# Kernel tuning notes

Hardware: AMD Instinct MI355X
Metric: run time of the kernel (lower is better)

The kernel has to match this reference:

```python
import jax, jax.numpy as jnp
import numpy as np
from jax.scipy.special import logsumexp

S, L = 32768, 512  # seq_len, label_num


def setup_inputs() -> dict:
    key = jax.random.key(0)
    k1, k2, k3 = jax.random.split(key, 3)
    logit = jax.random.normal(k1, (S, L), dtype=jnp.float32)   # emissions [S, L]
    labels = jax.random.randint(k2, (S,), 0, L)                # gold path [S]
    T = jax.random.normal(k3, (L, L), dtype=jnp.float32)       # T[next, prev]
    return {"logit": logit, "labels": labels, "T": T}


def _crf_loss(logit, T, labels):
    # Forward algorithm: alpha_t[j] = logsumexp_i(alpha_{t-1}[i] + T[j, i]) + feat_t[j]
    alpha0 = logit[0]

    def step(alpha, feat):
        new_alpha = logsumexp(alpha[None, :] + T, axis=1) + feat  # [L]
        return new_alpha, None

    alpha_final, _ = jax.lax.scan(step, alpha0, logit[1:])
    log_Z = logsumexp(alpha_final)

    # Gold path score: feat_0[y0] + sum_{t>0} (feat_t[y_t] + T[y_t, y_{t-1}])
    emit = logit[0, labels[0]] + jnp.sum(logit[jnp.arange(1, logit.shape[0]), labels[1:]])
    trans = jnp.sum(T[labels[1:], labels[:-1]])
    gold = emit + trans
    return log_Z - gold


def reference(logit, labels, T):
    return _crf_loss(logit, T, labels)
```

## Files before the change

kernel.cpp:

```cpp
#include <hip/hip_runtime.h>
#include <stdint.h>


#define S_LEN 32768
#define L 512
#define CH 16
#define NCF 2048
#define NB  256
#define LN448 6.104793232f
#define LN2   0.6931471806f

#define OFF_EAF  0
#define OFF_EAB  (256*1024)
#define OFF_G    (512*1024)
#define OFF_H    (OFF_G + 2048*512*2)
#define OFF_LSE  (OFF_H + 2048*512*2)
#define OFF_GOLD (OFF_LSE + 4104*4)
#define OFF_BAR  (OFF_GOLD + 1024)

typedef float v4f __attribute__((ext_vector_type(4)));

__device__ __forceinline__ float b2f(unsigned short u){
  return __uint_as_float(((unsigned)u) << 16);
}
__device__ __forceinline__ unsigned short f2b(float x){
  unsigned u = __float_as_uint(x);
  return (unsigned short)((u + 0x7fffu + ((u >> 16) & 1u)) >> 16);
}
__device__ __forceinline__ unsigned char to_fp8(float v){
  int u = __builtin_amdgcn_cvt_pk_fp8_f32(v, v, 0, false);
  return (unsigned char)(u & 0xff);
}

__device__ __forceinline__ void stg_u8(unsigned char* p, unsigned char v){
  __hip_atomic_store(p, v, __ATOMIC_RELAXED, __HIP_MEMORY_SCOPE_AGENT);
}
__device__ __forceinline__ void stg_u64(unsigned long long* p, unsigned long long v){
  __hip_atomic_store(p, v, __ATOMIC_RELAXED, __HIP_MEMORY_SCOPE_AGENT);
}
__device__ __forceinline__ void stg_f32(float* p, float v){
  __hip_atomic_store(p, v, __ATOMIC_RELAXED, __HIP_MEMORY_SCOPE_AGENT);
}

__device__ __forceinline__ void grid_bar(unsigned* bar, unsigned target){
  __syncthreads();
  if (threadIdx.x == 0) {
    __hip_atomic_fetch_add(bar, 1u, __ATOMIC_RELAXED, __HIP_MEMORY_SCOPE_AGENT);
    unsigned it = 0;
    while (__hip_atomic_load(bar, __ATOMIC_RELAXED, __HIP_MEMORY_SCOPE_AGENT) < target) {
      __builtin_amdgcn_s_sleep(8);
      if ((++it & 255u) == 0u)
        (void)__hip_atomic_load(bar, __ATOMIC_ACQUIRE, __HIP_MEMORY_SCOPE_AGENT);
    }
    __builtin_amdgcn_fence(__ATOMIC_ACQUIRE, "agent");
  }
  __syncthreads();
}

__device__ __forceinline__ float blockSum(float v, float* sred){
  #pragma unroll
  for (int off = 32; off >= 1; off >>= 1) v += __shfl_xor(v, off);
  int wid = threadIdx.x >> 6, lane = threadIdx.x & 63;
  if (lane == 0) sred[wid] = v;
  __syncthreads();
  if (threadIdx.x < 8) {
    float t = sred[threadIdx.x];
    t += __shfl_xor(t, 4); t += __shfl_xor(t, 2); t += __shfl_xor(t, 1);
    if (threadIdx.x == 0) sred[15] = t;
  }
  __syncthreads();
  float r = sred[15];
  __syncthreads();
  return r;
}

__device__ __forceinline__ float waveMax(float v){
  #pragma unroll
  for (int off = 32; off >= 1; off >>= 1) v = fmaxf(v, __shfl_xor(v, off));
  return v;
}
__device__ __forceinline__ float waveSum(float v){
  #pragma unroll
  for (int off = 32; off >= 1; off >>= 1) v += __shfl_xor(v, off);
  return v;
}

extern "C" __global__ __launch_bounds__(512, 2)
void crf_fused(const float* __restrict__ logit,
               const int* __restrict__ labels,
               const float* __restrict__ T,
               float* __restrict__ out,
               unsigned char* __restrict__ EAf,
               unsigned char* __restrict__ EAb,
               unsigned short* __restrict__ G,
               unsigned short* __restrict__ H,
               float* __restrict__ lsebuf,
               float* __restrict__ part,
               unsigned* __restrict__ bar){
  __shared__ __align__(16) unsigned char Pl[2][8192];
  __shared__ float sPart[16][8];
  __shared__ float sredG[16];

  const int tidx = threadIdx.x;

  for (int tid = blockIdx.x*512 + tidx; tid < 262144; tid += NB*512) {
    int r    = tid & 7;
    int lane = (tid >> 3) & 63;
    int kt   = (tid >> 9) & 15;
    int mtw  = tid >> 13;
    int j = (mtw >> 2)*64 + (mtw & 3)*16 + (lane & 15);
    int i = kt*32 + ((lane >> 4) << 3) + r;
    stg_u8(EAf + tid, to_fp8(2.0f * __expf(T[j*L + i])));
    stg_u8(EAb + tid, to_fp8(2.0f * __expf(T[i*L + j])));
  }
  {
    float acc = 0.f;
    if (tidx < 128) {
      int t = blockIdx.x*128 + tidx;
      int yt = labels[t];
      float v = logit[(size_t)t*L + yt];
      if (t > 0) v += T[yt*L + labels[t-1]];
      acc = v;
    }
    float s = blockSum(acc, sredG);
    if (tidx == 0) stg_f32(part + blockIdx.x, s);
  }
  grid_bar(bar, NB);

  {
    const int w    = tidx >> 6;
    const int lane = tidx & 63;
    const int quad = lane >> 4;
    const int cl   = lane & 15;
    const bool fwd = (blockIdx.x < NB/2);
    const int  b   = fwd ? blockIdx.x : (blockIdx.x - NB/2);
    const int  cg  = fwd ? (b*16 + cl) : (1 + b*16 + cl);
    const int  cgc = min(cg, NCF-1);
    const bool isc0 = fwd && (cg == 0);
    const int  jrow0 = w*64 + quad*4;

    const long* EA = (const long*)(fwd ? EAf : EAb);
    long eA[4][16];
    #pragma unroll
    for (int mt = 0; mt < 4; ++mt)
      #pragma unroll
      for (int kt = 0; kt < 16; ++kt)
        eA[mt][kt] = EA[(((w<<2)+mt)<<4 | kt)*64 + lane];

    float vr[4][4];
    if (fwd) {
      #pragma unroll
      for (int mt = 0; mt < 4; ++mt)
        #pragma unroll
        for (int r = 0; r < 4; ++r) vr[mt][r] = 1.0f;
    } else {
      const int t0 = cgc*CH + CH - 1;
      const float* lp = logit + (size_t)t0*L + jrow0;
      #pragma unroll
      for (int mt = 0; mt < 4; ++mt) {
        float4 x = *(const float4*)(lp + mt*16);
        vr[mt][0] = __expf(x.x); vr[mt][1] = __expf(x.y);
        vr[mt][2] = __expf(x.z); vr[mt][3] = __expf(x.w);
      }
    }
    float m = 0.0f;
    int par = 0;

    auto renorm_store = [&](int dst){
      float mx = vr[0][0];
      #pragma unroll
      for (int mt = 0; mt < 4; ++mt)
        #pragma unroll
        for (int r = 0; r < 4; ++r) mx = fmaxf(mx, vr[mt][r]);
      mx = fmaxf(mx, __shfl_xor(mx, 16));
      mx = fmaxf(mx, __shfl_xor(mx, 32));
      if (quad == 0) sPart[cl][w] = mx;
      __syncthreads();
      float4 pa = *(const float4*)&sPart[cl][0];
      float4 pb = *(const float4*)&sPart[cl][4];
      float M = fmaxf(fmaxf(fmaxf(pa.x,pa.y),fmaxf(pa.z,pa.w)),
                      fmaxf(fmaxf(pb.x,pb.y),fmaxf(pb.z,pb.w)));
      float sc = 448.0f / M;
      #pragma unroll
      for (int mt = 0; mt < 4; ++mt) {
        int u = __builtin_amdgcn_cvt_pk_fp8_f32(vr[mt][0]*sc, vr[mt][1]*sc, 0, false);
        u     = __builtin_amdgcn_cvt_pk_fp8_f32(vr[mt][2]*sc, vr[mt][3]*sc, u, true);
        int r0 = jrow0 + mt*16;
        *(int*)&Pl[dst][(r0 >> 5)*512 + ((((r0 >> 3) & 3)*16 + cl) << 3) + (r0 & 7)] = u;
      }
      m += __logf(M) - LN448;
      __syncthreads();
    };

    renorm_store(0);

    for (int k = 0; k < CH; ++k) {
      const bool last = (k == CH-1);
      const bool useF = fwd || !last;

      float4 pf[4];
      if (useF) {
        const int t = fwd ? (cgc*CH + k) : (cgc*CH + CH - 2 - k);
        const float* lp = logit + (size_t)t*L + jrow0;
        #pragma unroll
        for (int mt = 0; mt < 4; ++mt) pf[mt] = *(const float4*)(lp + mt*16);
      }

      v4f acc[4];
      #pragma unroll
      for (int mt = 0; mt < 4; ++mt) acc[mt] = (v4f){0.f,0.f,0.f,0.f};
      #pragma unroll
      for (int kt = 0; kt < 16; ++kt) {
        long bb = *(const long*)&Pl[par][kt*512 + lane*8];
        #pragma unroll
        for (int mt = 0; mt < 4; ++mt)
          acc[mt] = __builtin_amdgcn_mfma_f32_16x16x32_fp8_fp8(eA[mt][kt], bb, acc[mt], 0, 0, 0);
      }
      m -= LN2;

      if (useF) {
        #pragma unroll
        for (int mt = 0; mt < 4; ++mt) {
          float f0 = __expf(pf[mt].x), f1 = __expf(pf[mt].y);
          float f2 = __expf(pf[mt].z), f3 = __expf(pf[mt].w);
          vr[mt][0] = acc[mt][0]*f0; vr[mt][1] = acc[mt][1]*f1;
          vr[mt][2] = acc[mt][2]*f2; vr[mt][3] = acc[mt][3]*f3;
          if (k == 0 && isc0) {
            vr[mt][0] = f0; vr[mt][1] = f1; vr[mt][2] = f2; vr[mt][3] = f3;
          }
        }
        if (k == 0 && isc0) m = 0.0f;
      } else {
        #pragma unroll
        for (int mt = 0; mt < 4; ++mt)
          #pragma unroll
          for (int r = 0; r < 4; ++r) vr[mt][r] = acc[mt][r];
      }

      if (last) {
        if (cg <= NCF-1) {
          unsigned short* dst = (fwd ? G : H) + (size_t)cg*L + jrow0;
          #pragma unroll
          for (int mt = 0; mt < 4; ++mt) {
            unsigned long long pv =
                 (unsigned long long)f2b(__logf(vr[mt][0]) + m)
              | ((unsigned long long)f2b(__logf(vr[mt][1]) + m) << 16)
              | ((unsigned long long)f2b(__logf(vr[mt][2]) + m) << 32)
              | ((unsigned long long)f2b(__logf(vr[mt][3]) + m) << 48);
            stg_u64((unsigned long long*)(dst + mt*16), pv);
          }
        }
      } else {
        renorm_store(par ^ 1);
        par ^= 1;
      }
    }
  }
  grid_bar(bar, 2*NB);

  {
    const int w    = tidx >> 6;
    const int lane = tidx & 63;
    const int g    = blockIdx.x*8 + w;
    const int j8   = lane*8;
    if (g == 0) {
      const unsigned short* p = G + (size_t)(NCF-1)*L + j8;
      ushort4 a = *(const ushort4*)p, b = *(const ushort4*)(p + 4);
      float v[8] = { b2f(a.x),b2f(a.y),b2f(a.z),b2f(a.w),
                     b2f(b.x),b2f(b.y),b2f(b.z),b2f(b.w) };
      float mx = v[0];
      #pragma unroll
      for (int r = 1; r < 8; ++r) mx = fmaxf(mx, v[r]);
      mx = waveMax(mx);
      float s = 0.f;
      #pragma unroll
      for (int r = 0; r < 8; ++r) s += __expf(v[r] - mx);
      s = waveSum(s);
      if (lane == 0) stg_f32(lsebuf + 2*NCF, mx + __logf(s));
    } else {
      const unsigned short* hp = H + (size_t)g*L + j8;
      const unsigned short* gp = G + (size_t)(g-1)*L + j8;
      ushort4 ha = *(const ushort4*)hp, hb = *(const ushort4*)(hp + 4);
      ushort4 ga = *(const ushort4*)gp, gb = *(const ushort4*)(gp + 4);
      float hv[8] = { b2f(ha.x),b2f(ha.y),b2f(ha.z),b2f(ha.w),
                      b2f(hb.x),b2f(hb.y),b2f(hb.z),b2f(hb.w) };
      float gv[8] = { b2f(ga.x),b2f(ga.y),b2f(ga.z),b2f(ga.w),
                      b2f(gb.x),b2f(gb.y),b2f(gb.z),b2f(gb.w) };
      float m1 = -3.0e38f, m2 = -3.0e38f;
      #pragma unroll
      for (int r = 0; r < 8; ++r) {
        float a = hv[r] + gv[r];
        m1 = fmaxf(m1, a); m2 = fmaxf(m2, hv[r]);
      }
      m1 = waveMax(m1); m2 = waveMax(m2);
      float s1 = 0.f, s2 = 0.f;
      #pragma unroll
      for (int r = 0; r < 8; ++r) {
        s1 += __expf(hv[r] + gv[r] - m1);
        s2 += __expf(hv[r] - m2);
      }
      s1 = waveSum(s1); s2 = waveSum(s2);
      if (lane == 0) {
        stg_f32(lsebuf + g,       m1 + __logf(s1));
        stg_f32(lsebuf + NCF + g, m2 + __logf(s2));
      }
    }
  }
  grid_bar(bar, 3*NB);

  if (blockIdx.x == 0) {
    float acc = 0.f;
    for (int c = tidx; c < NCF; c += 512)
      if (c >= 1) acc += lsebuf[c] - lsebuf[NCF + c];
    if (tidx < NB) acc -= part[tidx];
    float s = blockSum(acc, sredG);
    if (tidx == 0) out[0] = lsebuf[2*NCF] + s;
  }
}

extern "C" void kernel_launch(void* const* d_in, const int* in_sizes, int n_in,
                              void* d_out, int out_size, void* d_ws, size_t ws_size,
                              hipStream_t stream){
  const float* logit = (const float*)d_in[0];
  const int* labels  = (const int*)d_in[1];
  const float* T     = (const float*)d_in[2];
  char* ws = (char*)d_ws;

  hipMemsetAsync(ws + OFF_BAR, 0, 64, stream);
  crf_fused<<<NB, 512, 0, stream>>>(
      logit, labels, T, (float*)d_out,
      (unsigned char*)(ws + OFF_EAF), (unsigned char*)(ws + OFF_EAB),
      (unsigned short*)(ws + OFF_G), (unsigned short*)(ws + OFF_H),
      (float*)(ws + OFF_LSE), (float*)(ws + OFF_GOLD),
      (unsigned*)(ws + OFF_BAR));
}
```

Measured before the change: 163.8 us.

## Double block size to 16 waves, halving per-wave MFMA tiles in chunk scan

Raises threads per block from 512 to 1024 so each of the 16 waves owns two 16-row MFMA tiles instead of four. The aim is to shorten the serial per-step MFMA and exp chain inside each chunk by spreading it over more waves. It also prefetches the next step's emission row during the current step, and replaces __syncthreads with a raw s_barrier after an LDS wait. The cost is a wider cross-wave max reduction, more barrier participants, and register-pressure limits from launch bounds (1024,4).

```diff
diff --git a/kernel.cpp b/kernel.cpp
--- a/kernel.cpp
+++ b/kernel.cpp
@@ -7,6 +7,7 @@
 #define CH 16
 #define NCF 2048
 #define NB  256
+#define TPB 1024
 #define LN448 6.104793232f
 #define LN2   0.6931471806f
 
@@ -42,6 +43,13 @@
   __hip_atomic_store(p, v, __ATOMIC_RELAXED, __HIP_MEMORY_SCOPE_AGENT);
 }
 
+__device__ __forceinline__ void lds_sync(){
+  asm volatile("s_waitcnt lgkmcnt(0)" ::: "memory");
+  __builtin_amdgcn_sched_barrier(0);
+  __builtin_amdgcn_s_barrier();
+  __builtin_amdgcn_sched_barrier(0);
+}
+
 __device__ __forceinline__ void grid_bar(unsigned* bar, unsigned target){
   __syncthreads();
   if (threadIdx.x == 0) {
@@ -63,13 +71,14 @@
   int wid = threadIdx.x >> 6, lane = threadIdx.x & 63;
   if (lane == 0) sred[wid] = v;
   __syncthreads();
-  if (threadIdx.x < 8) {
+  if (threadIdx.x < 16) {
     float t = sred[threadIdx.x];
-    t += __shfl_xor(t, 4); t += __shfl_xor(t, 2); t += __shfl_xor(t, 1);
-    if (threadIdx.x == 0) sred[15] = t;
-  }
-  __syncthreads();
-  float r = sred[15];
+    t += __shfl_xor(t, 8); t += __shfl_xor(t, 4);
+    t += __shfl_xor(t, 2); t += __shfl_xor(t, 1);
+    if (threadIdx.x == 0) sred[16] = t;
+  }
+  __syncthreads();
+  float r = sred[16];
   __syncthreads();
   return r;
 }
@@ -85,7 +94,7 @@
   return v;
 }
 
-extern "C" __global__ __launch_bounds__(512, 2)
+extern "C" __global__ __launch_bounds__(TPB, 4)
 void crf_fused(const float* __restrict__ logit,
                const int* __restrict__ labels,
                const float* __restrict__ T,
@@ -97,18 +106,19 @@
                float* __restrict__ lsebuf,
                float* __restrict__ part,
                unsigned* __restrict__ bar){
-  __shared__ __align__(16) unsigned char Pl[2][8192];
-  __shared__ float sPart[16][8];
-  __shared__ float sredG[16];
+  __shared__ __align__(16) unsigned char Pl[2*8192];
+  __shared__ float sPart[16][20];
+  __shared__ float sredG[17];
 
   const int tidx = threadIdx.x;
 
-  for (int tid = blockIdx.x*512 + tidx; tid < 262144; tid += NB*512) {
+  {
+    int tid = blockIdx.x*TPB + tidx;
     int r    = tid & 7;
     int lane = (tid >> 3) & 63;
     int kt   = (tid >> 9) & 15;
-    int mtw  = tid >> 13;
-    int j = (mtw >> 2)*64 + (mtw & 3)*16 + (lane & 15);
+    int R16  = tid >> 13;
+    int j = R16*16 + (lane & 15);
     int i = kt*32 + ((lane >> 4) << 3) + r;
     stg_u8(EAf + tid, to_fp8(2.0f * __expf(T[j*L + i])));
     stg_u8(EAb + tid, to_fp8(2.0f * __expf(T[i*L + j])));
@@ -137,59 +147,70 @@
     const int  cg  = fwd ? (b*16 + cl) : (1 + b*16 + cl);
     const int  cgc = min(cg, NCF-1);
     const bool isc0 = fwd && (cg == 0);
-    const int  jrow0 = w*64 + quad*4;
+    const int  jrow0 = w*32 + quad*4;
 
     const long* EA = (const long*)(fwd ? EAf : EAb);
-    long eA[4][16];
+    long eA[2][16];
     #pragma unroll
-    for (int mt = 0; mt < 4; ++mt)
+    for (int mt = 0; mt < 2; ++mt)
       #pragma unroll
       for (int kt = 0; kt < 16; ++kt)
-        eA[mt][kt] = EA[(((w<<2)+mt)<<4 | kt)*64 + lane];
-
-    float vr[4][4];
+        eA[mt][kt] = EA[(((w*2 + mt)*16) + kt)*64 + lane];
+
+    int pladdr[2];
+    #pragma unroll
+    for (int mt = 0; mt < 2; ++mt) {
+      int r0 = jrow0 + mt*16;
+      pladdr[mt] = (r0 >> 5)*512 + ((((r0 >> 3) & 3)*16 + cl) << 3) + (r0 & 7);
+    }
+    const int bbbase = lane*8;
+
+    const int tstart = fwd ? (cgc*CH) : (cgc*CH + CH - 2);
+    const int dstep  = fwd ? L : -L;
+    const float* lp = logit + (size_t)tstart*L + jrow0;
+    float4 pf0, pf1;
+
+    float vr[2][4];
     if (fwd) {
       #pragma unroll
-      for (int mt = 0; mt < 4; ++mt)
+      for (int mt = 0; mt < 2; ++mt)
         #pragma unroll
         for (int r = 0; r < 4; ++r) vr[mt][r] = 1.0f;
     } else {
-      const int t0 = cgc*CH + CH - 1;
-      const float* lp = logit + (size_t)t0*L + jrow0;
-      #pragma unroll
-      for (int mt = 0; mt < 4; ++mt) {
-        float4 x = *(const float4*)(lp + mt*16);
-        vr[mt][0] = __expf(x.x); vr[mt][1] = __expf(x.y);
-        vr[mt][2] = __expf(x.z); vr[mt][3] = __expf(x.w);
-      }
+      const float* ip = logit + (size_t)(cgc*CH + CH - 1)*L + jrow0;
+      float4 x0 = *(const float4*)ip, x1 = *(const float4*)(ip + 16);
+      vr[0][0] = __expf(x0.x); vr[0][1] = __expf(x0.y);
+      vr[0][2] = __expf(x0.z); vr[0][3] = __expf(x0.w);
+      vr[1][0] = __expf(x1.x); vr[1][1] = __expf(x1.y);
+      vr[1][2] = __expf(x1.z); vr[1][3] = __expf(x1.w);
     }
     float m = 0.0f;
     int par = 0;
 
+    pf0 = *(const float4*)lp; pf1 = *(const float4*)(lp + 16);
+
     auto renorm_store = [&](int dst){
-      float mx = vr[0][0];
-      #pragma unroll
-      for (int mt = 0; mt < 4; ++mt)
-        #pragma unroll
-        for (int r = 0; r < 4; ++r) mx = fmaxf(mx, vr[mt][r]);
+      float mx = fmaxf(fmaxf(fmaxf(vr[0][0],vr[0][1]), fmaxf(vr[0][2],vr[0][3])),
+                       fmaxf(fmaxf(vr[1][0],vr[1][1]), fmaxf(vr[1][2],vr[1][3])));
       mx = fmaxf(mx, __shfl_xor(mx, 16));
       mx = fmaxf(mx, __shfl_xor(mx, 32));
       if (quad == 0) sPart[cl][w] = mx;
-      __syncthreads();
-      float4 pa = *(const float4*)&sPart[cl][0];
-      float4 pb = *(const float4*)&sPart[cl][4];
-      float M = fmaxf(fmaxf(fmaxf(pa.x,pa.y),fmaxf(pa.z,pa.w)),
-                      fmaxf(fmaxf(pb.x,pb.y),fmaxf(pb.z,pb.w)));
+      lds_sync();
+      const float4* sp = (const float4*)&sPart[cl][0];
+      float4 a0 = sp[0], a1 = sp[1], a2 = sp[2], a3 = sp[3];
+      float M = fmaxf(fmaxf(fmaxf(fmaxf(a0.x,a0.y),fmaxf(a0.z,a0.w)),
+                            fmaxf(fmaxf(a1.x,a1.y),fmaxf(a1.z,a1.w))),
+                      fmaxf(fmaxf(fmaxf(a2.x,a2.y),fmaxf(a2.z,a2.w)),
+                            fmaxf(fmaxf(a3.x,a3.y),fmaxf(a3.z,a3.w))));
       float sc = 448.0f / M;
       #pragma unroll
-      for (int mt = 0; mt < 4; ++mt) {
+      for (int mt = 0; mt < 2; ++mt) {
         int u = __builtin_amdgcn_cvt_pk_fp8_f32(vr[mt][0]*sc, vr[mt][1]*sc, 0, false);
         u     = __builtin_amdgcn_cvt_pk_fp8_f32(vr[mt][2]*sc, vr[mt][3]*sc, u, true);
-        int r0 = jrow0 + mt*16;
-        *(int*)&Pl[dst][(r0 >> 5)*512 + ((((r0 >> 3) & 3)*16 + cl) << 3) + (r0 & 7)] = u;
+        *(int*)&Pl[dst*8192 + pladdr[mt]] = u;
       }
       m += __logf(M) - LN448;
-      __syncthreads();
+      lds_sync();
     };
 
     renorm_store(0);
@@ -198,50 +219,49 @@
       const bool last = (k == CH-1);
       const bool useF = fwd || !last;
 
-      float4 pf[4];
+      v4f acc0 = (v4f){0.f,0.f,0.f,0.f};
+      v4f acc1 = (v4f){0.f,0.f,0.f,0.f};
+      {
+        const unsigned char* plr = &Pl[par*8192 + bbbase];
+        #pragma unroll
+        for (int kt = 0; kt < 16; ++kt) {
+          long bb = *(const long*)(plr + kt*512);
+          acc0 = __builtin_amdgcn_mfma_f32_16x16x32_fp8_fp8(eA[0][kt], bb, acc0, 0, 0, 0);
+          acc1 = __builtin_amdgcn_mfma_f32_16x16x32_fp8_fp8(eA[1][kt], bb, acc1, 0, 0, 0);
+        }
+      }
+      m -= LN2;
+
       if (useF) {
-        const int t = fwd ? (cgc*CH + k) : (cgc*CH + CH - 2 - k);
-        const float* lp = logit + (size_t)t*L + jrow0;
-        #pragma unroll
-        for (int mt = 0; mt < 4; ++mt) pf[mt] = *(const float4*)(lp + mt*16);
-      }
-
-      v4f acc[4];
-      #pragma unroll
-      for (int mt = 0; mt < 4; ++mt) acc[mt] = (v4f){0.f,0.f,0.f,0.f};
-      #pragma unroll
-      for (int kt = 0; kt < 16; ++kt) {
-        long bb = *(const long*)&Pl[par][kt*512 + lane*8];
-        #pragma unroll
-        for (int mt = 0; mt < 4; ++mt)
-          acc[mt] = __builtin_amdgcn_mfma_f32_16x16x32_fp8_fp8(eA[mt][kt], bb, acc[mt], 0, 0, 0);
-      }
-      m -= LN2;
-
-      if (useF) {
-        #pragma unroll
-        for (int mt = 0; mt < 4; ++mt) {
-          float f0 = __expf(pf[mt].x), f1 = __expf(pf[mt].y);
-          float f2 = __expf(pf[mt].z), f3 = __expf(pf[mt].w);
-          vr[mt][0] = acc[mt][0]*f0; vr[mt][1] = acc[mt][1]*f1;
-          vr[mt][2] = acc[mt][2]*f2; vr[mt][3] = acc[mt][3]*f3;
-          if (k == 0 && isc0) {
-            vr[mt][0] = f0; vr[mt][1] = f1; vr[mt][2] = f2; vr[mt][3] = f3;
-          }
+        float f0 = __expf(pf0.x), f1 = __expf(pf0.y);
+        float f2 = __expf(pf0.z), f3 = __expf(pf0.w);
+        float g0 = __expf(pf1.x), g1 = __expf(pf1.y);
+        float g2 = __expf(pf1.z), g3 = __expf(pf1.w);
+        vr[0][0] = acc0[0]*f0; vr[0][1] = acc0[1]*f1;
+        vr[0][2] = acc0[2]*f2; vr[0][3] = acc0[3]*f3;
+        vr[1][0] = acc1[0]*g0; vr[1][1] = acc1[1]*g1;
+        vr[1][2] = acc1[2]*g2; vr[1][3] = acc1[3]*g3;
+        if (k == 0 && isc0) {
+          vr[0][0] = f0; vr[0][1] = f1; vr[0][2] = f2; vr[0][3] = f3;
+          vr[1][0] = g0; vr[1][1] = g1; vr[1][2] = g2; vr[1][3] = g3;
+          m = 0.0f;
         }
-        if (k == 0 && isc0) m = 0.0f;
       } else {
-        #pragma unroll
-        for (int mt = 0; mt < 4; ++mt)
-          #pragma unroll
-          for (int r = 0; r < 4; ++r) vr[mt][r] = acc[mt][r];
+        vr[0][0] = acc0[0]; vr[0][1] = acc0[1]; vr[0][2] = acc0[2]; vr[0][3] = acc0[3];
+        vr[1][0] = acc1[0]; vr[1][1] = acc1[1]; vr[1][2] = acc1[2]; vr[1][3] = acc1[3];
+      }
+
+      const bool nextF = fwd ? (k+1 < CH) : (k+1 < CH-1);
+      if (nextF) {
+        lp += dstep;
+        pf0 = *(const float4*)lp; pf1 = *(const float4*)(lp + 16);
       }
 
       if (last) {
         if (cg <= NCF-1) {
           unsigned short* dst = (fwd ? G : H) + (size_t)cg*L + jrow0;
           #pragma unroll
-          for (int mt = 0; mt < 4; ++mt) {
+          for (int mt = 0; mt < 2; ++mt) {
             unsigned long long pv =
                  (unsigned long long)f2b(__logf(vr[mt][0]) + m)
               | ((unsigned long long)f2b(__logf(vr[mt][1]) + m) << 16)
@@ -258,16 +278,16 @@
   }
   grid_bar(bar, 2*NB);
 
-  {
+  if (blockIdx.x < 128) {
     const int w    = tidx >> 6;
     const int lane = tidx & 63;
-    const int g    = blockIdx.x*8 + w;
+    const int g    = blockIdx.x*16 + w;
     const int j8   = lane*8;
     if (g == 0) {
       const unsigned short* p = G + (size_t)(NCF-1)*L + j8;
-      ushort4 a = *(const ushort4*)p, b = *(const ushort4*)(p + 4);
+      ushort4 a = *(const ushort4*)p, bq = *(const ushort4*)(p + 4);
       float v[8] = { b2f(a.x),b2f(a.y),b2f(a.z),b2f(a.w),
-                     b2f(b.x),b2f(b.y),b2f(b.z),b2f(b.w) };
+                     b2f(bq.x),b2f(bq.y),b2f(bq.z),b2f(bq.w) };
       float mx = v[0];
       #pragma unroll
       for (int r = 1; r < 8; ++r) mx = fmaxf(mx, v[r]);
@@ -310,7 +330,7 @@
 
   if (blockIdx.x == 0) {
     float acc = 0.f;
-    for (int c = tidx; c < NCF; c += 512)
+    for (int c = tidx; c < NCF; c += TPB)
       if (c >= 1) acc += lsebuf[c] - lsebuf[NCF + c];
     if (tidx < NB) acc -= part[tidx];
     float s = blockSum(acc, sredG);
@@ -327,7 +347,7 @@
   char* ws = (char*)d_ws;
 
   hipMemsetAsync(ws + OFF_BAR, 0, 64, stream);
-  crf_fused<<<NB, 512, 0, stream>>>(
+  crf_fused<<<NB, TPB, 0, stream>>>(
       logit, labels, T, (float*)d_out,
       (unsigned char*)(ws + OFF_EAF), (unsigned char*)(ws + OFF_EAB),
       (unsigned short*)(ws + OFF_G), (unsigned short*)(ws + OFF_H),
```

New measurement: 152.0 us. 1.08x faster.
